# Performance work log

Hardware: AMD Instinct MI355X
Metric: run time of the kernel (lower is better)

## Reference

```python
import jax, jax.numpy as jnp
import numpy as np

B, S, E, NH = 2, 2048, 1024, 16
THETA = 10000.0


def setup_inputs() -> dict:
    key = jax.random.key(0)
    k1, k2 = jax.random.split(key, 2)
    hidden_states = jax.random.normal(k1, (B, S, E), dtype=jnp.float32)
    in_proj_weight = jax.random.normal(k2, (3 * E, E), dtype=jnp.float32) * 0.02
    in_proj_bias = jnp.zeros((3 * E,), dtype=jnp.float32)
    return {
        "hidden_states": hidden_states,
        "in_proj_weight": in_proj_weight,
        "in_proj_bias": in_proj_bias,
        "T": 1,
        "H": 32,
        "W": 64,
    }


def _rope(x, cos, sin):
    # x: [BT, seq, n_heads, head_dim]; cos/sin: [seq, head_dim//2]
    # pairs are consecutive elements (x[2i], x[2i+1]) == complex (re, im)
    xr = x.reshape(x.shape[:-1] + (-1, 2))
    xe, xo = xr[..., 0], xr[..., 1]
    c = cos[None, :, None, :]
    s = sin[None, :, None, :]
    re = xe * c - xo * s
    im = xe * s + xo * c
    return jnp.stack([re, im], axis=-1).reshape(x.shape)


def reference(hidden_states, in_proj_weight, in_proj_bias, T, H, W):
    Bx, Sx, Ex = hidden_states.shape
    hd = Ex // NH
    # fused QKV projection
    qkv = hidden_states @ in_proj_weight.T + in_proj_bias
    q, k, v = jnp.split(qkv, 3, axis=-1)
    # 1D rotary over chunks of length S//T (T=1 -> full sequence)
    seq = Sx // T
    inv_freq = 1.0 / (THETA ** (jnp.arange(0, hd, 2, dtype=jnp.float32) / hd))
    ang = jnp.arange(seq, dtype=jnp.float32)[:, None] * inv_freq  # [seq, hd//2]
    cos, sin = jnp.cos(ang), jnp.sin(ang)
    q = _rope(q.reshape(Bx * T, seq, NH, hd), cos, sin).reshape(Bx, Sx, NH, hd)
    k = _rope(k.reshape(Bx * T, seq, NH, hd), cos, sin).reshape(Bx, Sx, NH, hd)
    v = v.reshape(Bx, Sx, NH, hd)
    # scaled dot-product attention (special_attn encoder path: no out_proj)
    scale = 1.0 / jnp.sqrt(jnp.asarray(hd, dtype=jnp.float32))
    scores = jnp.einsum('bqnd,bknd->bnqk', q, k) * scale
    attn = jax.nn.softmax(scores, axis=-1)
    out = jnp.einsum('bnqk,bknd->bqnd', attn, v)
    return out.reshape(Bx, Sx, Ex)
```

## Files before the change

kernel.cpp:

```cpp
#include <hip/hip_runtime.h>
#include <math.h>

#define BB 2
#define SS 2048
#define EE 1024
#define NHH 16
#define HD 64
#define HD2 32

typedef _Float16 f16x8 __attribute__((ext_vector_type(8)));
typedef __attribute__((ext_vector_type(4))) float f32x4;

static __device__ __forceinline__ unsigned pkh(float a, float b) {
    union { _Float16 h[2]; unsigned u; } v;
    v.h[0] = (_Float16)a; v.h[1] = (_Float16)b;
    return v.u;
}

static __device__ __forceinline__ void dma16(const void* g, void* l) {
    __builtin_amdgcn_global_load_lds(
        (const __attribute__((address_space(1))) unsigned int*)g,
        (__attribute__((address_space(3))) unsigned int*)l,
        16, 0, 0);
}

#define NXCHUNK 524288
#define NWCHUNK 393216
__global__ __launch_bounds__(256) void tabcvt_k(
    const float* __restrict__ X, const float* __restrict__ W,
    unsigned short* __restrict__ Xh, unsigned short* __restrict__ Wh,
    float* __restrict__ ct, float* __restrict__ st)
{
    int bid = blockIdx.x;
    if (bid < 256) {
        int idx = bid * 256 + threadIdx.x;
        int s = idx >> 5, p = idx & 31;
        double inv = pow(10000.0, -(double)(2 * p) / 64.0);
        double ang = (double)s * inv;
        ct[idx] = (float)cos(ang);
        st[idx] = (float)sin(ang);
        return;
    }
    int idx = (bid - 256) * 256 + threadIdx.x;
    const float* src;
    unsigned short* dst;
    int c;
    if (idx < NXCHUNK) { src = X; dst = Xh; c = idx; }
    else               { src = W; dst = Wh; c = idx - NXCHUNK;
                         if (c >= NWCHUNK) return; }
    int l15 = c & 15, q = (c >> 4) & 3, grp = (c >> 6) & 7;
    int kt = (c >> 9) & 31, t = c >> 14;
    int row = t * 128 + grp * 16 + l15;
    int k   = kt * 32 + q * 8;
    float4 v0 = *(const float4*)(src + (size_t)row * EE + k);
    float4 v1 = *(const float4*)(src + (size_t)row * EE + k + 4);
    *(uint4*)(dst + (size_t)c * 8) =
        make_uint4(pkh(v0.x, v0.y), pkh(v0.z, v0.w), pkh(v1.x, v1.y), pkh(v1.z, v1.w));
}

__global__ __launch_bounds__(256, 3) void qkv_mfma_k(
    const unsigned short* __restrict__ Xh, const unsigned short* __restrict__ Wh,
    const float* __restrict__ bias,
    const float* __restrict__ ct, const float* __restrict__ st,
    unsigned short* __restrict__ Qg, unsigned short* __restrict__ Kg,
    unsigned short* __restrict__ Vg)
{
    __shared__ __align__(16) unsigned short Alds[2][4096];
    __shared__ __align__(16) unsigned short Blds[2][4096];

    const int tid  = threadIdx.x;
    const int wave = tid >> 6;
    const int lane = tid & 63;
    const int quad = lane >> 4;
    const int l15  = lane & 15;

    const int id    = blockIdx.x;
    const int xcd   = id & 7;
    const int local = id >> 3;
    const int nt    = xcd * 3 + local % 3;
    const int mt    = local / 3;
    const int m0    = mt * 128;
    const int n0b   = nt * 128;

    f32x4 acc[4][4];
#pragma unroll
    for (int mc = 0; mc < 4; mc++)
#pragma unroll
        for (int nc = 0; nc < 4; nc++) acc[mc][nc] = (f32x4){0.f, 0.f, 0.f, 0.f};

    const int mg = (wave >> 1) * 4;
    const int ng = (wave & 1) * 4;

    {
        const unsigned short* at = Xh + ((size_t)(mt * 32)) * 4096;
        const unsigned short* bt = Wh + ((size_t)(nt * 32)) * 4096;
        dma16(at + (size_t)tid * 8,         &Alds[0][tid * 8]);
        dma16(at + (size_t)(tid + 256) * 8, &Alds[0][(tid + 256) * 8]);
        dma16(bt + (size_t)tid * 8,         &Blds[0][tid * 8]);
        dma16(bt + (size_t)(tid + 256) * 8, &Blds[0][(tid + 256) * 8]);
    }
    __syncthreads();

    int cur = 0;
    for (int kt = 0; kt < EE / 32; kt++) {
        if (kt + 1 < EE / 32) {
            const unsigned short* at = Xh + ((size_t)(mt * 32 + kt + 1)) * 4096;
            const unsigned short* bt = Wh + ((size_t)(nt * 32 + kt + 1)) * 4096;
            dma16(at + (size_t)tid * 8,         &Alds[cur ^ 1][tid * 8]);
            dma16(at + (size_t)(tid + 256) * 8, &Alds[cur ^ 1][(tid + 256) * 8]);
            dma16(bt + (size_t)tid * 8,         &Blds[cur ^ 1][tid * 8]);
            dma16(bt + (size_t)(tid + 256) * 8, &Blds[cur ^ 1][(tid + 256) * 8]);
        }

        f16x8 Af[4], Bf[4];
#pragma unroll
        for (int mc = 0; mc < 4; mc++)
            Af[mc] = *(const f16x8*)(&Alds[cur][((mg + mc) * 4 + quad) * 128 + l15 * 8]);
#pragma unroll
        for (int nc = 0; nc < 4; nc++)
            Bf[nc] = *(const f16x8*)(&Blds[cur][((ng + nc) * 4 + quad) * 128 + l15 * 8]);
#pragma unroll
        for (int mc = 0; mc < 4; mc++)
#pragma unroll
            for (int nc = 0; nc < 4; nc++)
                acc[mc][nc] = __builtin_amdgcn_mfma_f32_16x16x32_f16(Af[mc], Bf[nc], acc[mc][nc], 0, 0, 0);

        __syncthreads();
        cur ^= 1;
    }

    const int n0w = n0b + (wave & 1) * 64;
    const int m0w = m0 + (wave >> 1) * 64;
    const int sec = n0w >> 10;
    const int h   = (n0w & 1023) >> 6;
    const int bq  = m0w >> 11;
    const size_t abase = (size_t)(bq * NHH + h) * 131072;
    unsigned short* dst = (sec == 0) ? Qg : (sec == 1) ? Kg : Vg;

    float bn[4];
#pragma unroll
    for (int nc = 0; nc < 4; nc++) bn[nc] = bias[n0w + nc * 16 + l15];

    if (sec < 2) {
        const float scq = (sec == 0) ? 0.18033688f : 1.0f;
#pragma unroll
        for (int mc = 0; mc < 4; mc++) {
            int sb = (m0w & 2047) + mc * 16;
#pragma unroll
            for (int nc = 0; nc < 4; nc++) {
                int d = nc * 16 + l15;
                int p = d >> 1;
                int kc_d = d >> 5, quad_a = (d >> 3) & 3, j = d & 7;
#pragma unroll
                for (int rr = 0; rr < 4; rr++) {
                    int srow = sb + quad * 4 + rr;
                    float x = acc[mc][nc][rr] + bn[nc];
                    float xp = __shfl_xor(x, 1);
                    float c = ct[srow * 32 + p], sn = st[srow * 32 + p];
                    float o = ((l15 & 1) == 0) ? (x * c - xp * sn) : (xp * sn + x * c);
                    o *= scq;
                    float op = __shfl_xor(o, 1);
                    if ((l15 & 1) == 0) {
                        unsigned u = pkh(o, op);
                        size_t e = abase +
                            (size_t)((((srow >> 4) * 2 + kc_d) * 4 + quad_a)) * 128 +
                            (srow & 15) * 8 + j;
                        *(unsigned int*)(dst + e) = u;
                    }
                }
            }
        }
    } else {
#pragma unroll
        for (int mc = 0; mc < 4; mc++) {
            int sb = (m0w & 2047) + mc * 16;
            int s32 = sb >> 5;
            int quad_v = ((sb >> 3) + (quad >> 1)) & 3;
            int j0 = (quad & 1) * 4;
#pragma unroll
            for (int nc = 0; nc < 4; nc++) {
                float x0 = acc[mc][nc][0] + bn[nc];
                float x1 = acc[mc][nc][1] + bn[nc];
                float x2 = acc[mc][nc][2] + bn[nc];
                float x3 = acc[mc][nc][3] + bn[nc];
                unsigned u01 = pkh(x0, x1), u23 = pkh(x2, x3);
                size_t e = abase +
                    (size_t)(((s32 * 4 + nc) * 4 + quad_v)) * 128 + l15 * 8 + j0;
                *(uint2*)(dst + e) = make_uint2(u01, u23);
            }
        }
    }
}

__global__ __launch_bounds__(256, 4) void attn_mfma_k(
    const unsigned short* __restrict__ Qg,
    const unsigned short* __restrict__ Kg,
    const unsigned short* __restrict__ Vg,
    float* __restrict__ out)
{
    __shared__ __align__(16) unsigned short Klds[2][8192];
    __shared__ __align__(16) unsigned short Pbuf[4][1024];

    const int tid  = threadIdx.x;
    const int wave = tid >> 6;
    const int lane = tid & 63;
    const int quad = lane >> 4;
    const int l15  = lane & 15;
    const int id   = blockIdx.x;
    const int bh   = (id & 7) * 4 + ((id >> 3) & 3);
    const int qt   = id >> 5;
    const int b    = bh >> 4, h = bh & 15;
    const int q0   = qt * 64 + wave * 16;
    const size_t abase = (size_t)bh * 131072;

    f16x8 qf[2];
#pragma unroll
    for (int kc = 0; kc < 2; kc++)
        qf[kc] = *(const f16x8*)(Qg + abase +
            (size_t)((((q0 >> 4) * 2 + kc) * 4 + quad)) * 128 + l15 * 8);

    f32x4 acc[4];
#pragma unroll
    for (int dc = 0; dc < 4; dc++) acc[dc] = (f32x4){0.f, 0.f, 0.f, 0.f};
    float mst = -INFINITY, lst = 0.f;

    const int laneoff = quad * 128 + l15 * 8;
    const unsigned short* kgb = Kg + abase;
    const unsigned short* vt0 = Vg + abase + laneoff;
    const unsigned short* vt1 = vt0 + 2048;
    unsigned short* Pw = Pbuf[wave];

    auto process64 = [&](const unsigned short* ktile) {
        f16x8 vf[4][2];
#pragma unroll
        for (int dc = 0; dc < 4; dc++) {
            vf[dc][0] = *(const f16x8*)(vt0 + dc * 512);
            vf[dc][1] = *(const f16x8*)(vt1 + dc * 512);
        }

        const unsigned short* kb = ktile + laneoff;
        f32x4 stt[4];
        __builtin_amdgcn_s_setprio(1);
#pragma unroll
        for (int mc = 0; mc < 4; mc++) {
            f16x8 a0 = *(const f16x8*)(kb + mc * 1024);
            f16x8 a1 = *(const f16x8*)(kb + mc * 1024 + 512);
            f32x4 s = (f32x4){0.f, 0.f, 0.f, 0.f};
            s = __builtin_amdgcn_mfma_f32_16x16x32_f16(a0, qf[0], s, 0, 0, 0);
            s = __builtin_amdgcn_mfma_f32_16x16x32_f16(a1, qf[1], s, 0, 0, 0);
            stt[mc] = s;
        }
        __builtin_amdgcn_s_setprio(0);

        float mt = -INFINITY;
#pragma unroll
        for (int mc = 0; mc < 4; mc++)
#pragma unroll
            for (int rr = 0; rr < 4; rr++) mt = fmaxf(mt, stt[mc][rr]);
        mt = fmaxf(mt, __shfl_xor(mt, 16));
        mt = fmaxf(mt, __shfl_xor(mt, 32));

        if (!__all(mt - mst <= 8.f)) {
            float mnew = fmaxf(mst, mt);
            float alpha = __builtin_amdgcn_exp2f(mst - mnew);
            lst *= alpha;
            float ar[4];
#pragma unroll
            for (int rr = 0; rr < 4; rr++)
                ar[rr] = __shfl(alpha, (lane & 48) + ((lane >> 4) << 2) + rr);
#pragma unroll
            for (int dc = 0; dc < 4; dc++)
#pragma unroll
                for (int rr = 0; rr < 4; rr++) acc[dc][rr] *= ar[rr];
            mst = mnew;
        }

        float ps = 0.f;
#pragma unroll
        for (int mc = 0; mc < 4; mc++) {
            float e0 = __builtin_amdgcn_exp2f(stt[mc][0] - mst);
            float e1 = __builtin_amdgcn_exp2f(stt[mc][1] - mst);
            float e2 = __builtin_amdgcn_exp2f(stt[mc][2] - mst);
            float e3 = __builtin_amdgcn_exp2f(stt[mc][3] - mst);
            ps += (e0 + e1) + (e2 + e3);
            int kk2 = mc >> 1;
            int quadp = (mc & 1) * 2 + (quad >> 1);
            int j0 = (quad & 1) * 4;
            *(uint2*)(Pw + (kk2 * 4 + quadp) * 128 + l15 * 8 + j0) =
                make_uint2(pkh(e0, e1), pkh(e2, e3));
        }
        ps += __shfl_xor(ps, 16);
        ps += __shfl_xor(ps, 32);
        lst += ps;

        f16x8 pf[2];
#pragma unroll
        for (int kk2 = 0; kk2 < 2; kk2++)
            pf[kk2] = *(const f16x8*)(Pw + (kk2 * 4 + quad) * 128 + l15 * 8);

        __builtin_amdgcn_s_setprio(1);
#pragma unroll
        for (int dc = 0; dc < 4; dc++) {
            f32x4 aa = acc[dc];
#pragma unroll
            for (int kk2 = 0; kk2 < 2; kk2++)
                aa = __builtin_amdgcn_mfma_f32_16x16x32_f16(pf[kk2], vf[dc][kk2], aa, 0, 0, 0);
            acc[dc] = aa;
        }
        __builtin_amdgcn_s_setprio(0);

        vt0 += 4096;
        vt1 += 4096;
    };

#pragma unroll
    for (int i = 0; i < 4; i++)
        dma16(kgb + (size_t)(tid + i * 256) * 8, &Klds[0][(tid + i * 256) * 8]);
    __syncthreads();

    int cur = 0;
    for (int it = 0; it < SS / 128; it++) {
        if (it + 1 < SS / 128) {
            const unsigned short* ks = kgb + (size_t)(it + 1) * 8192;
#pragma unroll
            for (int i = 0; i < 4; i++)
                dma16(ks + (size_t)(tid + i * 256) * 8,
                      &Klds[cur ^ 1][(tid + i * 256) * 8]);
        }

        process64(&Klds[cur][0]);
        process64(&Klds[cur][4096]);

        __syncthreads();
        cur ^= 1;
    }

    float linv = 1.f / lst;
    float lr[4];
#pragma unroll
    for (int rr = 0; rr < 4; rr++)
        lr[rr] = __shfl(linv, (lane & 48) + ((lane >> 4) << 2) + rr);
#pragma unroll
    for (int dc = 0; dc < 4; dc++)
#pragma unroll
        for (int rr = 0; rr < 4; rr++) {
            int s = q0 + quad * 4 + rr;
            out[((size_t)(b * SS + s)) * EE + h * HD + dc * 16 + l15] = acc[dc][rr] * lr[rr];
        }
}

extern "C" void kernel_launch(void* const* d_in, const int* in_sizes, int n_in,
                              void* d_out, int out_size, void* d_ws, size_t ws_size,
                              hipStream_t stream) {
    const float* X    = (const float*)d_in[0];
    const float* W    = (const float*)d_in[1];
    const float* bias = (const float*)d_in[2];
    float* out = (float*)d_out;

    float* ws = (float*)d_ws;
    float* ct = ws;
    float* st = ws + 65536;
    unsigned short* base = (unsigned short*)(ws + 131072);
    const size_t ASZ = (size_t)32 * 131072;
    unsigned short* Qg = base;
    unsigned short* Kg = base + ASZ;
    unsigned short* Vg = base + 2 * ASZ;
    unsigned short* Xh = base + 3 * ASZ;
    unsigned short* Wh = Xh + (size_t)NXCHUNK * 8;

    tabcvt_k<<<dim3(256 + (NXCHUNK + NWCHUNK) / 256), 256, 0, stream>>>(
        X, W, Xh, Wh, ct, st);
    qkv_mfma_k<<<dim3(768), 256, 0, stream>>>(
        Xh, Wh, bias, ct, st, Qg, Kg, Vg);
    attn_mfma_k<<<dim3(1024), 256, 0, stream>>>(Qg, Kg, Vg, out);
}
```

Baseline: 184.7 us.

## Permute K/V layouts so P stays in registers, removing LDS round-trip

The projection epilogue now writes K and V in a permuted key order, chosen so that the softmax probabilities each lane computes from the QK^T MFMA output line up with the A-operand layout needed by the PV MFMA. The per-wave P buffer in LDS and its write/read round-trip are removed, and packed fp16 probabilities are assembled directly in registers. The max reduction is also rebalanced into a tree. This relies on the key permutation being consistent across K, V and the score layout, and it changes global access patterns for V loads.

```diff
diff --git a/kernel.cpp b/kernel.cpp
--- a/kernel.cpp
+++ b/kernel.cpp
@@ -162,9 +162,18 @@
                     float op = __shfl_xor(o, 1);
                     if ((l15 & 1) == 0) {
                         unsigned u = pkh(o, op);
-                        size_t e = abase +
-                            (size_t)((((srow >> 4) * 2 + kc_d) * 4 + quad_a)) * 128 +
-                            (srow & 15) * 8 + j;
+                        size_t e;
+                        if (sec == 0) {
+                            e = abase +
+                                (size_t)((((srow >> 4) * 2 + kc_d) * 4 + quad_a)) * 128 +
+                                (srow & 15) * 8 + j;
+                        } else {
+                            int key6 = srow & 63;
+                            int mc_k = ((key6 >> 4) & 2) | ((key6 >> 2) & 1);
+                            int l15k = ((key6 >> 1) & 12) | (key6 & 3);
+                            e = abase + (size_t)(srow >> 6) * 4096 +
+                                (mc_k * 2 + kc_d) * 512 + (quad_a * 16 + l15k) * 8 + j;
+                        }
                         *(unsigned int*)(dst + e) = u;
                     }
                 }
@@ -173,10 +182,9 @@
     } else {
 #pragma unroll
         for (int mc = 0; mc < 4; mc++) {
-            int sb = (m0w & 2047) + mc * 16;
-            int s32 = sb >> 5;
-            int quad_v = ((sb >> 3) + (quad >> 1)) & 3;
-            int j0 = (quad & 1) * 4;
+            int key  = (m0w & 2047) + mc * 16 + quad * 4;
+            int tile = key >> 6;
+            int key6 = key & 63;
 #pragma unroll
             for (int nc = 0; nc < 4; nc++) {
                 float x0 = acc[mc][nc][0] + bn[nc];
@@ -184,8 +192,8 @@
                 float x2 = acc[mc][nc][2] + bn[nc];
                 float x3 = acc[mc][nc][3] + bn[nc];
                 unsigned u01 = pkh(x0, x1), u23 = pkh(x2, x3);
-                size_t e = abase +
-                    (size_t)(((s32 * 4 + nc) * 4 + quad_v)) * 128 + l15 * 8 + j0;
+                int d = nc * 16 + l15;
+                size_t e = abase + (size_t)tile * 4096 + d * 64 + key6;
                 *(uint2*)(dst + e) = make_uint2(u01, u23);
             }
         }
@@ -199,7 +207,6 @@
     float* __restrict__ out)
 {
     __shared__ __align__(16) unsigned short Klds[2][8192];
-    __shared__ __align__(16) unsigned short Pbuf[4][1024];
 
     const int tid  = threadIdx.x;
     const int wave = tid >> 6;
@@ -224,21 +231,18 @@
     for (int dc = 0; dc < 4; dc++) acc[dc] = (f32x4){0.f, 0.f, 0.f, 0.f};
     float mst = -INFINITY, lst = 0.f;
 
-    const int laneoff = quad * 128 + l15 * 8;
     const unsigned short* kgb = Kg + abase;
-    const unsigned short* vt0 = Vg + abase + laneoff;
-    const unsigned short* vt1 = vt0 + 2048;
-    unsigned short* Pw = Pbuf[wave];
+    const unsigned short* vtb = Vg + abase + l15 * 64 + quad * 8;
 
     auto process64 = [&](const unsigned short* ktile) {
         f16x8 vf[4][2];
 #pragma unroll
         for (int dc = 0; dc < 4; dc++) {
-            vf[dc][0] = *(const f16x8*)(vt0 + dc * 512);
-            vf[dc][1] = *(const f16x8*)(vt1 + dc * 512);
-        }
-
-        const unsigned short* kb = ktile + laneoff;
+            vf[dc][0] = *(const f16x8*)(vtb + dc * 1024);
+            vf[dc][1] = *(const f16x8*)(vtb + dc * 1024 + 32);
+        }
+
+        const unsigned short* kb = ktile + lane * 8;
         f32x4 stt[4];
         __builtin_amdgcn_s_setprio(1);
 #pragma unroll
@@ -252,11 +256,11 @@
         }
         __builtin_amdgcn_s_setprio(0);
 
-        float mt = -INFINITY;
-#pragma unroll
-        for (int mc = 0; mc < 4; mc++)
-#pragma unroll
-            for (int rr = 0; rr < 4; rr++) mt = fmaxf(mt, stt[mc][rr]);
+        float t0 = fmaxf(fmaxf(stt[0][0], stt[0][1]), fmaxf(stt[0][2], stt[0][3]));
+        float t1 = fmaxf(fmaxf(stt[1][0], stt[1][1]), fmaxf(stt[1][2], stt[1][3]));
+        float t2 = fmaxf(fmaxf(stt[2][0], stt[2][1]), fmaxf(stt[2][2], stt[2][3]));
+        float t3 = fmaxf(fmaxf(stt[3][0], stt[3][1]), fmaxf(stt[3][2], stt[3][3]));
+        float mt = fmaxf(fmaxf(t0, t1), fmaxf(t2, t3));
         mt = fmaxf(mt, __shfl_xor(mt, 16));
         mt = fmaxf(mt, __shfl_xor(mt, 32));
 
@@ -276,6 +280,7 @@
         }
 
         float ps = 0.f;
+        unsigned up[4][2];
 #pragma unroll
         for (int mc = 0; mc < 4; mc++) {
             float e0 = __builtin_amdgcn_exp2f(stt[mc][0] - mst);
@@ -283,34 +288,30 @@
             float e2 = __builtin_amdgcn_exp2f(stt[mc][2] - mst);
             float e3 = __builtin_amdgcn_exp2f(stt[mc][3] - mst);
             ps += (e0 + e1) + (e2 + e3);
-            int kk2 = mc >> 1;
-            int quadp = (mc & 1) * 2 + (quad >> 1);
-            int j0 = (quad & 1) * 4;
-            *(uint2*)(Pw + (kk2 * 4 + quadp) * 128 + l15 * 8 + j0) =
-                make_uint2(pkh(e0, e1), pkh(e2, e3));
+            up[mc][0] = pkh(e0, e1);
+            up[mc][1] = pkh(e2, e3);
         }
         ps += __shfl_xor(ps, 16);
         ps += __shfl_xor(ps, 32);
         lst += ps;
 
-        f16x8 pf[2];
-#pragma unroll
-        for (int kk2 = 0; kk2 < 2; kk2++)
-            pf[kk2] = *(const f16x8*)(Pw + (kk2 * 4 + quad) * 128 + l15 * 8);
+        union { unsigned u[4]; f16x8 h; } pc0, pc1;
+        pc0.u[0] = up[0][0]; pc0.u[1] = up[0][1];
+        pc0.u[2] = up[1][0]; pc0.u[3] = up[1][1];
+        pc1.u[0] = up[2][0]; pc1.u[1] = up[2][1];
+        pc1.u[2] = up[3][0]; pc1.u[3] = up[3][1];
 
         __builtin_amdgcn_s_setprio(1);
 #pragma unroll
         for (int dc = 0; dc < 4; dc++) {
             f32x4 aa = acc[dc];
-#pragma unroll
-            for (int kk2 = 0; kk2 < 2; kk2++)
-                aa = __builtin_amdgcn_mfma_f32_16x16x32_f16(pf[kk2], vf[dc][kk2], aa, 0, 0, 0);
+            aa = __builtin_amdgcn_mfma_f32_16x16x32_f16(pc0.h, vf[dc][0], aa, 0, 0, 0);
+            aa = __builtin_amdgcn_mfma_f32_16x16x32_f16(pc1.h, vf[dc][1], aa, 0, 0, 0);
             acc[dc] = aa;
         }
         __builtin_amdgcn_s_setprio(0);
 
-        vt0 += 4096;
-        vt1 += 4096;
+        vtb += 4096;
     };
 
 #pragma unroll
```

Result: slower. 247.8 us (+34.2%).
